# Performance work log

Measured on AMD Instinct MI355X. Metric: run time of the kernel, lower is better.

## Reference

```python
import jax, jax.numpy as jnp
import numpy as np

DIM = 2048
Q_C = 1536
KV_C = 512
H = 16
DH = 128
DR = 64
EPS = 1e-6
B = 4
T = 2048


def rmsnorm(x, g, eps=EPS):
    var = jnp.mean(x * x, axis=-1, keepdims=True)
    return x * jax.lax.rsqrt(var + eps) * g


def apply_rope(x, freqs_cis):
    # x: [B, t, h, d]; freqs_cis: [t, d//2, 2] (cos, sin)
    xs = x.reshape(*x.shape[:-1], -1, 2)
    x1, x2 = xs[..., 0], xs[..., 1]
    cos = freqs_cis[None, :, None, :, 0]
    sin = freqs_cis[None, :, None, :, 1]
    o1 = x1 * cos - x2 * sin
    o2 = x1 * sin + x2 * cos
    return jnp.stack([o1, o2], axis=-1).reshape(x.shape)


def setup_inputs() -> dict:
    key = jax.random.key(0)
    ks = jax.random.split(key, 12)
    s = lambda fan_in: 1.0 / np.sqrt(fan_in)
    inp = {}
    inp["x"] = jax.random.normal(ks[0], (B, T, DIM), dtype=jnp.float32)
    inp["start_pos"] = 0
    # rotary frequencies for decoupled dim
    inv_freq = 1.0 / (10000.0 ** (np.arange(0, DR, 2, dtype=np.float32) / DR))
    angles = np.arange(T, dtype=np.float32)[:, None] * inv_freq[None, :]  # [T, DR//2]
    inp["freqs_cis"] = jnp.asarray(np.stack([np.cos(angles), np.sin(angles)], axis=-1))
    # causal additive mask
    neg = jnp.float32(-1e9)
    inp["mask"] = jnp.where(jnp.tril(jnp.ones((T, T), dtype=bool)), 0.0, neg).astype(jnp.float32)
    # weights stored as (in, out)
    inp["W_dq"] = jax.random.normal(ks[1], (DIM, Q_C), dtype=jnp.float32) * s(DIM)
    inp["W_uq"] = jax.random.normal(ks[2], (Q_C, H * DH), dtype=jnp.float32) * s(Q_C)
    inp["W_dkv"] = jax.random.normal(ks[3], (DIM, KV_C), dtype=jnp.float32) * s(DIM)
    inp["W_uk"] = jax.random.normal(ks[4], (KV_C, H * DH), dtype=jnp.float32) * s(KV_C)
    inp["W_uv"] = jax.random.normal(ks[5], (KV_C, H * DH), dtype=jnp.float32) * s(KV_C)
    inp["W_qr"] = jax.random.normal(ks[6], (Q_C, H * DR), dtype=jnp.float32) * s(Q_C)
    inp["W_kr"] = jax.random.normal(ks[7], (DIM, DR), dtype=jnp.float32) * s(DIM)
    inp["W_o"] = jax.random.normal(ks[8], (H * DH, DIM), dtype=jnp.float32) * s(H * DH)
    inp["g_q"] = jnp.ones((Q_C,), dtype=jnp.float32)
    inp["g_kv"] = jnp.ones((KV_C,), dtype=jnp.float32)
    return inp


def reference(x, start_pos, freqs_cis, mask, W_dq, W_uq, W_dkv, W_uk, W_uv, W_qr, W_kr, W_o, g_q, g_kv):
    Bc, t, _ = x.shape
    q_c = rmsnorm(x @ W_dq, g_q)            # [B, t, Q_C]
    kv_c = rmsnorm(x @ W_dkv, g_kv)         # [B, t, KV_C]
    q_rope = (q_c @ W_qr).reshape(Bc, t, H, DR)
    q_rope = apply_rope(q_rope, freqs_cis)
    k_rope = apply_rope((x @ W_kr)[:, :, None, :], freqs_cis)  # [B, t, 1, DR]
    k_rope = jnp.broadcast_to(k_rope, (Bc, t, H, DR))
    q = (q_c @ W_uq).reshape(Bc, t, H, DH)
    k = (kv_c @ W_uk).reshape(Bc, t, H, DH)
    v = (kv_c @ W_uv).reshape(Bc, t, H, DH)
    q = jnp.concatenate([q, q_rope], axis=-1)  # [B, t, H, DH+DR]
    k = jnp.concatenate([k, k_rope], axis=-1)
    scale = 1.0 / np.sqrt(DH + DR)
    scores = jnp.einsum("bqhd,bkhd->bhqk", q, k) * scale + mask
    probs = jax.nn.softmax(scores, axis=-1)
    out = jnp.einsum("bhqk,bkhd->bqhd", probs, v).reshape(Bc, t, H * DH)
    return out @ W_o
```

## Files before the change

kernel.cpp:

```cpp
#include <hip/hip_runtime.h>
#include <cstdint>
#include <cstddef>

typedef unsigned short u16;
typedef __attribute__((ext_vector_type(8))) short s8v;
typedef __attribute__((ext_vector_type(4))) float f4v;

__device__ __forceinline__ float bf2f(u16 u) {
  union { unsigned u; float f; } v; v.u = ((unsigned)u) << 16; return v.f;
}
__device__ __forceinline__ u16 f2bf(float f) {
  union { float f; unsigned u; } v; v.f = f;
  unsigned r = v.u + 0x7FFFu + ((v.u >> 16) & 1u);
  return (u16)(r >> 16);
}

__device__ __forceinline__ void async16(u16* lds, const u16* g) {
  __builtin_amdgcn_global_load_lds((const __attribute__((address_space(1))) void*)g,
                                   (__attribute__((address_space(3))) void*)lds,
                                   16, 0, 0);
}

__global__ __launch_bounds__(256) void k_f32_to_bf16(const float* __restrict__ in,
                                                     u16* __restrict__ out, int n8) {
  int i = blockIdx.x * 256 + threadIdx.x;
  if (i >= n8) return;
  const float4* p = (const float4*)(in + (size_t)i * 8);
  float4 a = p[0], b = p[1];
  s8v ov;
  ov[0] = (short)f2bf(a.x); ov[1] = (short)f2bf(a.y);
  ov[2] = (short)f2bf(a.z); ov[3] = (short)f2bf(a.w);
  ov[4] = (short)f2bf(b.x); ov[5] = (short)f2bf(b.y);
  ov[6] = (short)f2bf(b.z); ov[7] = (short)f2bf(b.w);
  *(s8v*)(out + (size_t)i * 8) = ov;
}

__global__ __launch_bounds__(256) void k_transpose_bf16(const float* __restrict__ W,
                                                        u16* __restrict__ Wt, int K, int N) {
  __shared__ float tile[32][33];
  int n0 = blockIdx.x * 32, k0 = blockIdx.y * 32;
  int tx = threadIdx.x & 31, ty = threadIdx.x >> 5;
#pragma unroll
  for (int i = 0; i < 32; i += 8)
    tile[ty + i][tx] = W[(size_t)(k0 + ty + i) * N + n0 + tx];
  __syncthreads();
#pragma unroll
  for (int i = 0; i < 32; i += 8)
    Wt[(size_t)(n0 + ty + i) * K + k0 + tx] = f2bf(tile[tx][ty + i]);
}

template <int BM, int BN, int WVM, int WVN, typename OutT, bool REMAP>
__global__ __launch_bounds__(256, 2) void k_gemm_bt(const u16* __restrict__ A,
                                                    const u16* __restrict__ Bt,
                                                    OutT* __restrict__ C,
                                                    int M, int N, int K, int ldc) {
  constexpr int FM = BM / WVM / 16, FN = BN / WVN / 16;
  __shared__ __align__(16) u16 As[BM * 32];
  __shared__ __align__(16) u16 Bs[BN * 32];
  const int tid = threadIdx.x, wv = tid >> 6, ln = tid & 63;
  const int lo = ln & 15, hi = ln >> 4;
  const int wr = wv / WVN, wc = wv % WVN;

  int nwg = gridDim.x, bid = blockIdx.x;
  int s = (bid & 7) * (nwg >> 3) + (bid >> 3);
  int gm = M / BM;
  int m0 = (s % gm) * BM, n0 = (s / gm) * BN;

  f4v acc[FM][FN] = {};

  for (int k0 = 0; k0 < K; k0 += 32) {
    __syncthreads();
#pragma unroll
    for (int i = 0; i < BM / 64; i++) {
      int r = i * 64 + wv * 16 + (ln >> 2);
      async16(&As[(i * 64 + wv * 16) * 32],
              A + (size_t)(m0 + r) * K + k0 + (ln & 3) * 8);
    }
#pragma unroll
    for (int i = 0; i < BN / 64; i++) {
      int r = i * 64 + wv * 16 + (ln >> 2);
      async16(&Bs[(i * 64 + wv * 16) * 32],
              Bt + (size_t)(n0 + r) * K + k0 + (ln & 3) * 8);
    }
    __syncthreads();

    s8v af[FM], bf[FN];
#pragma unroll
    for (int m = 0; m < FM; m++)
      af[m] = *(const s8v*)&As[(wr * FM * 16 + m * 16 + lo) * 32 + hi * 8];
#pragma unroll
    for (int n = 0; n < FN; n++)
      bf[n] = *(const s8v*)&Bs[(wc * FN * 16 + n * 16 + lo) * 32 + hi * 8];
#pragma unroll
    for (int m = 0; m < FM; m++)
#pragma unroll
      for (int n = 0; n < FN; n++)
        acc[m][n] = __builtin_amdgcn_mfma_f32_16x16x32_bf16(af[m], bf[n], acc[m][n], 0, 0, 0);
  }

#pragma unroll
  for (int m = 0; m < FM; m++)
#pragma unroll
    for (int n = 0; n < FN; n++)
#pragma unroll
      for (int j = 0; j < 4; j++) {
        int row = m0 + wr * FM * 16 + m * 16 + hi * 4 + j;
        int col = n0 + wc * FN * 16 + n * 16 + lo;
        int dc = REMAP ? ((col >> 7) * 192 + (col & 127)) : col;
        float v = acc[m][n][j];
        if constexpr (sizeof(OutT) == 2)
          C[(size_t)row * ldc + dc] = (OutT)f2bf(v);
        else
          C[(size_t)row * ldc + dc] = (OutT)v;
      }
}

__global__ __launch_bounds__(256) void k_rmsnorm(u16* __restrict__ buf,
                                                 const float* __restrict__ g, int C) {
  int row = blockIdx.x;
  u16* p = buf + (size_t)row * C;
  int tid = threadIdx.x;
  bool act = tid * 8 < C;
  float x[8];
  float ss = 0.f;
  if (act) {
    s8v v = *(const s8v*)(p + tid * 8);
#pragma unroll
    for (int i = 0; i < 8; i++) { float xi = bf2f((u16)v[i]); x[i] = xi; ss += xi * xi; }
  }
#pragma unroll
  for (int off = 1; off < 64; off <<= 1) ss += __shfl_xor(ss, off);
  __shared__ float red[4];
  if ((tid & 63) == 0) red[tid >> 6] = ss;
  __syncthreads();
  float sc = rsqrtf((red[0] + red[1] + red[2] + red[3]) / (float)C + 1e-6f);
  if (act) {
    s8v ov;
#pragma unroll
    for (int i = 0; i < 8; i++) ov[i] = (short)f2bf(x[i] * sc * g[tid * 8 + i]);
    *(s8v*)(p + tid * 8) = ov;
  }
}

__global__ __launch_bounds__(256) void k_rope_q(const u16* __restrict__ qr,
                                                const float* __restrict__ freqs,
                                                u16* __restrict__ qbuf) {
  int idx = blockIdx.x * 256 + threadIdx.x;
  int r = idx >> 4, h = idx & 15;
  int t = r & 2047;
  const u16* src = qr + (size_t)r * 1024 + h * 64;
  u16* dst = qbuf + (size_t)r * 3072 + h * 192 + 128;
  const float* fc = freqs + (size_t)t * 64;
  u16 in[64], out[64];
#pragma unroll
  for (int c = 0; c < 8; c++) {
    s8v vv = *(const s8v*)(src + c * 8);
#pragma unroll
    for (int e = 0; e < 8; e++) in[c * 8 + e] = (u16)vv[e];
  }
#pragma unroll
  for (int i = 0; i < 32; i++) {
    float x1 = bf2f(in[2 * i]), x2 = bf2f(in[2 * i + 1]);
    float co = fc[2 * i], si = fc[2 * i + 1];
    out[2 * i] = f2bf(x1 * co - x2 * si);
    out[2 * i + 1] = f2bf(x1 * si + x2 * co);
  }
#pragma unroll
  for (int c = 0; c < 8; c++) {
    s8v ov;
#pragma unroll
    for (int e = 0; e < 8; e++) ov[e] = (short)out[c * 8 + e];
    *(s8v*)(dst + c * 8) = ov;
  }
}

__global__ __launch_bounds__(256) void k_rope_k(const u16* __restrict__ kr,
                                                const float* __restrict__ freqs,
                                                u16* __restrict__ kbuf) {
  int idx = blockIdx.x * 256 + threadIdx.x;
  int r = idx >> 4, h = idx & 15;
  int t = r & 2047;
  const u16* src = kr + (size_t)r * 64;
  u16* dst = kbuf + (size_t)r * 3072 + h * 192 + 128;
  const float* fc = freqs + (size_t)t * 64;
  u16 in[64], out[64];
#pragma unroll
  for (int c = 0; c < 8; c++) {
    s8v vv = *(const s8v*)(src + c * 8);
#pragma unroll
    for (int e = 0; e < 8; e++) in[c * 8 + e] = (u16)vv[e];
  }
#pragma unroll
  for (int i = 0; i < 32; i++) {
    float x1 = bf2f(in[2 * i]), x2 = bf2f(in[2 * i + 1]);
    float co = fc[2 * i], si = fc[2 * i + 1];
    out[2 * i] = f2bf(x1 * co - x2 * si);
    out[2 * i + 1] = f2bf(x1 * si + x2 * co);
  }
#pragma unroll
  for (int c = 0; c < 8; c++) {
    s8v ov;
#pragma unroll
    for (int e = 0; e < 8; e++) ov[e] = (short)out[c * 8 + e];
    *(s8v*)(dst + c * 8) = ov;
  }
}

__global__ __launch_bounds__(256) void k_transpose_v(const u16* __restrict__ vtmp,
                                                     u16* __restrict__ vt) {
  __shared__ __align__(16) u16 tile[64][72];
  int r0 = blockIdx.x * 64, c0 = blockIdx.y * 64;
  int b = r0 >> 11, t0 = r0 & 2047;
  int h = c0 >> 7, d0 = c0 & 127;
  int tid = threadIdx.x;
  int ci = (tid & 7) * 8, ri = tid >> 3;
#pragma unroll
  for (int i = 0; i < 2; i++)
    *(s8v*)&tile[ri + 32 * i][ci] =
        *(const s8v*)(vtmp + (size_t)(r0 + ri + 32 * i) * 2048 + c0 + ci);
  __syncthreads();
  int tx = tid & 7, rr = tid >> 3;
#pragma unroll
  for (int i = 0; i < 2; i++) {
    int dr = rr + 32 * i;
    s8v ov;
#pragma unroll
    for (int e = 0; e < 8; e++) ov[e] = (short)tile[tx * 8 + e][dr];
    *(s8v*)(vt + (size_t)((b * 16 + h) * 128 + d0 + dr) * 2048 + t0 + tx * 8) = ov;
  }
}

__global__ __launch_bounds__(256, 3) void k_attn(const u16* __restrict__ Q,
                                                 const u16* __restrict__ K,
                                                 const u16* __restrict__ V,
                                                 u16* __restrict__ O) {
  __shared__ __align__(16) u16 Ks[64 * 192];
  __shared__ __align__(16) u16 Vs[128 * 64];
  __shared__ __align__(16) u16 p_lds[4][16 * 88];
  int bid = blockIdx.x;
  int lw = (bid & 7) * 256 + (bid >> 3);
  int qt = 31 - (lw & 31), h = (lw >> 5) & 15, b = lw >> 9;
  int tid = threadIdx.x, wv = tid >> 6, ln = tid & 63;
  int lo = ln & 15, hi = ln >> 4, lo7 = lo & 7;
  int qb = qt * 64 + wv * 16;

  const u16* qptr = Q + (size_t)(b * 2048 + qb + lo) * 3072 + h * 192 + hi * 8;
  s8v qf[6];
#pragma unroll
  for (int ks = 0; ks < 6; ks++) qf[ks] = *(const s8v*)(qptr + ks * 32);

  f4v Oa[8] = {};
  float m_r[4], l_r[4];
#pragma unroll
  for (int j = 0; j < 4; j++) { m_r[j] = -3e38f; l_r[j] = 0.f; }
  const float scale = 0.07216878364870323f;

  const u16* kg = K + (size_t)(b * 2048) * 3072 + h * 192;
  const u16* vg = V + (size_t)((b * 16 + h) * 128) * 2048;
  int kgo[6], klo[6];
#pragma unroll
  for (int i = 0; i < 6; i++) {
    int id = i * 256 + tid, r = id / 24, c = id % 24;
    kgo[i] = r * 3072 + c * 8;
    klo[i] = r * 192 + (c ^ (r & 7)) * 8;
  }
  int vgo[4], vlo[4];
#pragma unroll
  for (int i = 0; i < 4; i++) {
    int id = i * 256 + tid, r = id >> 3, c = id & 7;
    vgo[i] = r * 2048 + c * 8;
    vlo[i] = r * 64 + (c ^ (r & 7)) * 8;
  }

  u16* pl = p_lds[wv];
  int last = (qb + 15) >> 6;
  s8v kreg[6], vreg[4];

#pragma unroll
  for (int i = 0; i < 6; i++) kreg[i] = *(const s8v*)(kg + kgo[i]);
#pragma unroll
  for (int i = 0; i < 4; i++) vreg[i] = *(const s8v*)(vg + vgo[i]);
#pragma unroll
  for (int i = 0; i < 6; i++) *(s8v*)&Ks[klo[i]] = kreg[i];
#pragma unroll
  for (int i = 0; i < 4; i++) *(s8v*)&Vs[vlo[i]] = vreg[i];
  __syncthreads();

  for (int t = 0; t <= last; t++) {
    int kv0 = t * 64;
    if (t < last) {
      size_t ksh = (size_t)(kv0 + 64) * 3072;
#pragma unroll
      for (int i = 0; i < 6; i++) kreg[i] = *(const s8v*)(kg + ksh + kgo[i]);
#pragma unroll
      for (int i = 0; i < 4; i++) vreg[i] = *(const s8v*)(vg + (kv0 + 64) + vgo[i]);
    }

    f4v S[4] = {};
#pragma unroll
    for (int ks = 0; ks < 6; ks++)
#pragma unroll
      for (int nf = 0; nf < 4; nf++) {
        s8v kf = *(const s8v*)&Ks[(nf * 16 + lo) * 192 + (((ks * 4 + hi) ^ lo7) * 8)];
        S[nf] = __builtin_amdgcn_mfma_f32_16x16x32_bf16(qf[ks], kf, S[nf], 0, 0, 0);
      }

    float p[4][4], tmax[4];
#pragma unroll
    for (int j = 0; j < 4; j++) tmax[j] = -3e38f;
    bool diag = (t == last);
#pragma unroll
    for (int nf = 0; nf < 4; nf++)
#pragma unroll
      for (int j = 0; j < 4; j++) {
        float sv = S[nf][j] * scale;
        if (diag && (kv0 + nf * 16 + lo > qb + hi * 4 + j)) sv = -3e38f;
        p[nf][j] = sv;
        tmax[j] = fmaxf(tmax[j], sv);
      }
#pragma unroll
    for (int off = 1; off < 16; off <<= 1)
#pragma unroll
      for (int j = 0; j < 4; j++) tmax[j] = fmaxf(tmax[j], __shfl_xor(tmax[j], off));
    float fj[4], ts[4];
#pragma unroll
    for (int j = 0; j < 4; j++) {
      float nm = fmaxf(m_r[j], tmax[j]);
      fj[j] = __expf(m_r[j] - nm);
      m_r[j] = nm;
      ts[j] = 0.f;
    }
#pragma unroll
    for (int nf = 0; nf < 4; nf++)
#pragma unroll
      for (int j = 0; j < 4; j++) {
        float pv = __expf(p[nf][j] - m_r[j]);
        p[nf][j] = pv;
        ts[j] += pv;
      }
#pragma unroll
    for (int off = 1; off < 16; off <<= 1)
#pragma unroll
      for (int j = 0; j < 4; j++) ts[j] += __shfl_xor(ts[j], off);
#pragma unroll
    for (int j = 0; j < 4; j++) l_r[j] = l_r[j] * fj[j] + ts[j];
#pragma unroll
    for (int df = 0; df < 8; df++)
#pragma unroll
      for (int j = 0; j < 4; j++) Oa[df][j] *= fj[j];

#pragma unroll
    for (int nf = 0; nf < 4; nf++)
#pragma unroll
      for (int j = 0; j < 4; j++)
        pl[(hi * 4 + j) * 88 + nf * 16 + lo] = f2bf(p[nf][j]);

#pragma unroll
    for (int ks2 = 0; ks2 < 2; ks2++) {
      s8v pa = *(const s8v*)&pl[lo * 88 + ks2 * 32 + hi * 8];
#pragma unroll
      for (int df = 0; df < 8; df++) {
        s8v vf = *(const s8v*)&Vs[(df * 16 + lo) * 64 + (((ks2 * 4 + hi) ^ lo7) * 8)];
        Oa[df] = __builtin_amdgcn_mfma_f32_16x16x32_bf16(pa, vf, Oa[df], 0, 0, 0);
      }
    }

    __syncthreads();
    if (t < last) {
#pragma unroll
      for (int i = 0; i < 6; i++) *(s8v*)&Ks[klo[i]] = kreg[i];
#pragma unroll
      for (int i = 0; i < 4; i++) *(s8v*)&Vs[vlo[i]] = vreg[i];
      __syncthreads();
    }
  }

#pragma unroll
  for (int j = 0; j < 4; j++) {
    float inv = 1.0f / l_r[j];
    u16* orow = O + (size_t)(b * 2048 + qb + hi * 4 + j) * 2048 + h * 128;
#pragma unroll
    for (int df = 0; df < 8; df++) orow[df * 16 + lo] = f2bf(Oa[df][j] * inv);
  }
}

extern "C" void kernel_launch(void* const* d_in, const int* in_sizes, int n_in,
                              void* d_out, int out_size, void* d_ws, size_t ws_size,
                              hipStream_t stream) {
  (void)in_sizes; (void)n_in; (void)out_size; (void)ws_size;
  const float* x     = (const float*)d_in[0];
  const float* freqs = (const float*)d_in[2];
  const float* W_dq  = (const float*)d_in[4];
  const float* W_uq  = (const float*)d_in[5];
  const float* W_dkv = (const float*)d_in[6];
  const float* W_uk  = (const float*)d_in[7];
  const float* W_uv  = (const float*)d_in[8];
  const float* W_qr  = (const float*)d_in[9];
  const float* W_kr  = (const float*)d_in[10];
  const float* W_o   = (const float*)d_in[11];
  const float* g_q   = (const float*)d_in[12];
  const float* g_kv  = (const float*)d_in[13];
  float* out = (float*)d_out;

  const int M = 8192;
  char* w = (char*)d_ws;
  auto alloc = [&](size_t n) { char* p = w; w += (n + 255) & ~(size_t)255; return p; };

  u16* xb     = (u16*)alloc((size_t)M * 2048 * 2);
  u16* wdq    = (u16*)alloc((size_t)1536 * 2048 * 2);
  u16* wuq    = (u16*)alloc((size_t)2048 * 1536 * 2);
  u16* wdkv   = (u16*)alloc((size_t)512 * 2048 * 2);
  u16* wuk    = (u16*)alloc((size_t)2048 * 512 * 2);
  u16* wuv    = (u16*)alloc((size_t)2048 * 512 * 2);
  u16* wqr    = (u16*)alloc((size_t)1024 * 1536 * 2);
  u16* wkr    = (u16*)alloc((size_t)64 * 2048 * 2);
  u16* wo     = (u16*)alloc((size_t)2048 * 2048 * 2);
  u16* q_c    = (u16*)alloc((size_t)M * 1536 * 2);
  u16* kv_c   = (u16*)alloc((size_t)M * 512 * 2);
  u16* qr_raw = (u16*)alloc((size_t)M * 1024 * 2);
  u16* kr_raw = (u16*)alloc((size_t)M * 64 * 2);
  u16* qbuf   = (u16*)alloc((size_t)M * 3072 * 2);
  u16* kbuf   = (u16*)alloc((size_t)M * 3072 * 2);
  u16* vt     = (u16*)alloc((size_t)M * 2048 * 2);
  u16* vtmp = xb;
  u16* aout = xb;

  k_f32_to_bf16<<<M * 2048 / 8 / 256, 256, 0, stream>>>(x, xb, M * 2048 / 8);
  k_transpose_bf16<<<dim3(1536 / 32, 2048 / 32), 256, 0, stream>>>(W_dq, wdq, 2048, 1536);
  k_transpose_bf16<<<dim3(2048 / 32, 1536 / 32), 256, 0, stream>>>(W_uq, wuq, 1536, 2048);
  k_transpose_bf16<<<dim3(512 / 32, 2048 / 32), 256, 0, stream>>>(W_dkv, wdkv, 2048, 512);
  k_transpose_bf16<<<dim3(2048 / 32, 512 / 32), 256, 0, stream>>>(W_uk, wuk, 512, 2048);
  k_transpose_bf16<<<dim3(2048 / 32, 512 / 32), 256, 0, stream>>>(W_uv, wuv, 512, 2048);
  k_transpose_bf16<<<dim3(1024 / 32, 1536 / 32), 256, 0, stream>>>(W_qr, wqr, 1536, 1024);
  k_transpose_bf16<<<dim3(64 / 32, 2048 / 32), 256, 0, stream>>>(W_kr, wkr, 2048, 64);
  k_transpose_bf16<<<dim3(2048 / 32, 2048 / 32), 256, 0, stream>>>(W_o, wo, 2048, 2048);

  k_gemm_bt<128, 128, 2, 2, u16, false><<<(M / 128) * (1536 / 128), 256, 0, stream>>>(
      xb, wdq, q_c, M, 1536, 2048, 1536);
  k_rmsnorm<<<M, 256, 0, stream>>>(q_c, g_q, 1536);
  k_gemm_bt<128, 128, 2, 2, u16, false><<<(M / 128) * (512 / 128), 256, 0, stream>>>(
      xb, wdkv, kv_c, M, 512, 2048, 512);
  k_rmsnorm<<<M, 256, 0, stream>>>(kv_c, g_kv, 512);

  k_gemm_bt<128, 128, 2, 2, u16, true><<<(M / 128) * (2048 / 128), 256, 0, stream>>>(
      q_c, wuq, qbuf, M, 2048, 1536, 3072);
  k_gemm_bt<128, 128, 2, 2, u16, false><<<(M / 128) * (1024 / 128), 256, 0, stream>>>(
      q_c, wqr, qr_raw, M, 1024, 1536, 1024);
  k_rope_q<<<M * 16 / 256, 256, 0, stream>>>(qr_raw, freqs, qbuf);

  k_gemm_bt<128, 128, 2, 2, u16, true><<<(M / 128) * (2048 / 128), 256, 0, stream>>>(
      kv_c, wuk, kbuf, M, 2048, 512, 3072);
  k_gemm_bt<128, 64, 4, 1, u16, false><<<(M / 128) * (64 / 64), 256, 0, stream>>>(
      xb, wkr, kr_raw, M, 64, 2048, 64);
  k_rope_k<<<M * 16 / 256, 256, 0, stream>>>(kr_raw, freqs, kbuf);

  k_gemm_bt<128, 128, 2, 2, u16, false><<<(M / 128) * (2048 / 128), 256, 0, stream>>>(
      kv_c, wuv, vtmp, M, 2048, 512, 2048);
  k_transpose_v<<<dim3(M / 64, 2048 / 64), 256, 0, stream>>>(vtmp, vt);

  k_attn<<<4 * 16 * 32, 256, 0, stream>>>(qbuf, kbuf, vt, aout);

  k_gemm_bt<128, 128, 2, 2, float, false><<<(M / 128) * (2048 / 128), 256, 0, stream>>>(
      aout, wo, out, M, 2048, 2048, 2048);
}
```

Measured before the change: 839.0 us.

## Fuse sibling projection GEMMs and add lazy softmax rescaling in attention

Sibling projection GEMMs that share an input are merged into one launch by laying out their transposed weights next to each other (W_dq+W_dkv, W_uq+W_qr, W_uk+W_uv). A split-column epilogue routes each output half to its own buffer, which cuts launches and re-reads of the shared input. The attention kernel folds the scale into an exp2 multiplier, skips the rescale of the running max and accumulator unless the tile max grows past a threshold, and defers the row-sum reduction to the end. It also raises wave priority around the MFMA blocks. RMSNorm now launches with exactly C/8 threads, and bf16 conversion uses the library intrinsic; the lazy rescale can lose some precision if scores vary widely.

```diff
diff --git a/kernel.cpp b/kernel.cpp
--- a/kernel.cpp
+++ b/kernel.cpp
@@ -1,4 +1,5 @@
 #include <hip/hip_runtime.h>
+#include <hip/hip_bf16.h>
 #include <cstdint>
 #include <cstddef>
 
@@ -10,9 +11,8 @@
   union { unsigned u; float f; } v; v.u = ((unsigned)u) << 16; return v.f;
 }
 __device__ __forceinline__ u16 f2bf(float f) {
-  union { float f; unsigned u; } v; v.f = f;
-  unsigned r = v.u + 0x7FFFu + ((v.u >> 16) & 1u);
-  return (u16)(r >> 16);
+  __hip_bfloat16 h = __float2bfloat16(f);
+  return *reinterpret_cast<u16*>(&h);
 }
 
 __device__ __forceinline__ void async16(u16* lds, const u16* g) {
@@ -49,11 +49,12 @@
     Wt[(size_t)(n0 + ty + i) * K + k0 + tx] = f2bf(tile[tx][ty + i]);
 }
 
-template <int BM, int BN, int WVM, int WVN, typename OutT, bool REMAP>
-__global__ __launch_bounds__(256, 2) void k_gemm_bt(const u16* __restrict__ A,
-                                                    const u16* __restrict__ Bt,
-                                                    OutT* __restrict__ C,
-                                                    int M, int N, int K, int ldc) {
+template <int BM, int BN, int WVM, int WVN, int EPI>
+__global__ __launch_bounds__(256, 2) void k_gemm(const u16* __restrict__ A,
+                                                 const u16* __restrict__ Bt,
+                                                 void* __restrict__ C0v,
+                                                 void* __restrict__ C1v,
+                                                 int M, int N, int K, int split) {
   constexpr int FM = BM / WVM / 16, FN = BN / WVN / 16;
   __shared__ __align__(16) u16 As[BM * 32];
   __shared__ __align__(16) u16 Bs[BN * 32];
@@ -98,6 +99,7 @@
         acc[m][n] = __builtin_amdgcn_mfma_f32_16x16x32_bf16(af[m], bf[n], acc[m][n], 0, 0, 0);
   }
 
+  bool second = (n0 >= split);
 #pragma unroll
   for (int m = 0; m < FM; m++)
 #pragma unroll
@@ -106,40 +108,45 @@
       for (int j = 0; j < 4; j++) {
         int row = m0 + wr * FM * 16 + m * 16 + hi * 4 + j;
         int col = n0 + wc * FN * 16 + n * 16 + lo;
-        int dc = REMAP ? ((col >> 7) * 192 + (col & 127)) : col;
         float v = acc[m][n][j];
-        if constexpr (sizeof(OutT) == 2)
-          C[(size_t)row * ldc + dc] = (OutT)f2bf(v);
-        else
-          C[(size_t)row * ldc + dc] = (OutT)v;
+        if constexpr (EPI == 0) {
+          ((u16*)C0v)[(size_t)row * N + col] = f2bf(v);
+        } else if constexpr (EPI == 1) {
+          ((float*)C0v)[(size_t)row * N + col] = v;
+        } else if constexpr (EPI == 2) {
+          if (second) ((u16*)C1v)[(size_t)row * 512 + (col - 1536)] = f2bf(v);
+          else        ((u16*)C0v)[(size_t)row * 1536 + col] = f2bf(v);
+        } else if constexpr (EPI == 3) {
+          if (second) ((u16*)C1v)[(size_t)row * 1024 + (col - 2048)] = f2bf(v);
+          else        ((u16*)C0v)[(size_t)row * 3072 + (col >> 7) * 192 + (col & 127)] = f2bf(v);
+        } else {
+          if (second) ((u16*)C1v)[(size_t)row * 2048 + (col - 2048)] = f2bf(v);
+          else        ((u16*)C0v)[(size_t)row * 3072 + (col >> 7) * 192 + (col & 127)] = f2bf(v);
+        }
       }
 }
 
-__global__ __launch_bounds__(256) void k_rmsnorm(u16* __restrict__ buf,
-                                                 const float* __restrict__ g, int C) {
+__global__ void k_rmsnorm(u16* __restrict__ buf, const float* __restrict__ g, int C) {
   int row = blockIdx.x;
   u16* p = buf + (size_t)row * C;
   int tid = threadIdx.x;
-  bool act = tid * 8 < C;
   float x[8];
   float ss = 0.f;
-  if (act) {
-    s8v v = *(const s8v*)(p + tid * 8);
-#pragma unroll
-    for (int i = 0; i < 8; i++) { float xi = bf2f((u16)v[i]); x[i] = xi; ss += xi * xi; }
-  }
+  s8v v = *(const s8v*)(p + tid * 8);
+#pragma unroll
+  for (int i = 0; i < 8; i++) { float xi = bf2f((u16)v[i]); x[i] = xi; ss += xi * xi; }
 #pragma unroll
   for (int off = 1; off < 64; off <<= 1) ss += __shfl_xor(ss, off);
   __shared__ float red[4];
+  if (tid < 4) red[tid] = 0.f;
+  __syncthreads();
   if ((tid & 63) == 0) red[tid >> 6] = ss;
   __syncthreads();
   float sc = rsqrtf((red[0] + red[1] + red[2] + red[3]) / (float)C + 1e-6f);
-  if (act) {
-    s8v ov;
-#pragma unroll
-    for (int i = 0; i < 8; i++) ov[i] = (short)f2bf(x[i] * sc * g[tid * 8 + i]);
-    *(s8v*)(p + tid * 8) = ov;
-  }
+  s8v ov;
+#pragma unroll
+  for (int i = 0; i < 8; i++) ov[i] = (short)f2bf(x[i] * sc * g[tid * 8 + i]);
+  *(s8v*)(p + tid * 8) = ov;
 }
 
 __global__ __launch_bounds__(256) void k_rope_q(const u16* __restrict__ qr,
@@ -250,10 +257,11 @@
   for (int ks = 0; ks < 6; ks++) qf[ks] = *(const s8v*)(qptr + ks * 32);
 
   f4v Oa[8] = {};
-  float m_r[4], l_r[4];
-#pragma unroll
-  for (int j = 0; j < 4; j++) { m_r[j] = -3e38f; l_r[j] = 0.f; }
-  const float scale = 0.07216878364870323f;
+  float m_r[4], lpart[4];
+#pragma unroll
+  for (int j = 0; j < 4; j++) { m_r[j] = -3e38f; lpart[j] = 0.f; }
+  const float sl2 = 0.07216878364870323f * 1.44269504f;
+  const float THRU = 11.5f / sl2;
 
   const u16* kg = K + (size_t)(b * 2048) * 3072 + h * 192;
   const u16* vg = V + (size_t)((b * 16 + h) * 128) * 2048;
@@ -297,6 +305,7 @@
     }
 
     f4v S[4] = {};
+    __builtin_amdgcn_s_setprio(1);
 #pragma unroll
     for (int ks = 0; ks < 6; ks++)
 #pragma unroll
@@ -304,50 +313,56 @@
         s8v kf = *(const s8v*)&Ks[(nf * 16 + lo) * 192 + (((ks * 4 + hi) ^ lo7) * 8)];
         S[nf] = __builtin_amdgcn_mfma_f32_16x16x32_bf16(qf[ks], kf, S[nf], 0, 0, 0);
       }
+    __builtin_amdgcn_s_setprio(0);
 
     float p[4][4], tmax[4];
 #pragma unroll
     for (int j = 0; j < 4; j++) tmax[j] = -3e38f;
-    bool diag = (t == last);
+    if (t == last) {
+#pragma unroll
+      for (int nf = 0; nf < 4; nf++)
+#pragma unroll
+        for (int j = 0; j < 4; j++) {
+          float sv = S[nf][j];
+          if (kv0 + nf * 16 + lo > qb + hi * 4 + j) sv = -3e38f;
+          p[nf][j] = sv;
+          tmax[j] = fmaxf(tmax[j], sv);
+        }
+    } else {
+#pragma unroll
+      for (int nf = 0; nf < 4; nf++)
+#pragma unroll
+        for (int j = 0; j < 4; j++) {
+          p[nf][j] = S[nf][j];
+          tmax[j] = fmaxf(tmax[j], S[nf][j]);
+        }
+    }
+    bool need = false;
+#pragma unroll
+    for (int j = 0; j < 4; j++) need = need || (tmax[j] > m_r[j] + THRU);
+    if (__any(need)) {
+#pragma unroll
+      for (int off = 1; off < 16; off <<= 1)
+#pragma unroll
+        for (int j = 0; j < 4; j++) tmax[j] = fmaxf(tmax[j], __shfl_xor(tmax[j], off));
+#pragma unroll
+      for (int j = 0; j < 4; j++) {
+        float nm = fmaxf(m_r[j], tmax[j]);
+        float fj = exp2f((m_r[j] - nm) * sl2);
+        m_r[j] = nm;
+        lpart[j] *= fj;
+#pragma unroll
+        for (int df = 0; df < 8; df++) Oa[df][j] *= fj;
+      }
+    }
 #pragma unroll
     for (int nf = 0; nf < 4; nf++)
 #pragma unroll
       for (int j = 0; j < 4; j++) {
-        float sv = S[nf][j] * scale;
-        if (diag && (kv0 + nf * 16 + lo > qb + hi * 4 + j)) sv = -3e38f;
-        p[nf][j] = sv;
-        tmax[j] = fmaxf(tmax[j], sv);
+        float pv = exp2f((p[nf][j] - m_r[j]) * sl2);
+        p[nf][j] = pv;
+        lpart[j] += pv;
       }
-#pragma unroll
-    for (int off = 1; off < 16; off <<= 1)
-#pragma unroll
-      for (int j = 0; j < 4; j++) tmax[j] = fmaxf(tmax[j], __shfl_xor(tmax[j], off));
-    float fj[4], ts[4];
-#pragma unroll
-    for (int j = 0; j < 4; j++) {
-      float nm = fmaxf(m_r[j], tmax[j]);
-      fj[j] = __expf(m_r[j] - nm);
-      m_r[j] = nm;
-      ts[j] = 0.f;
-    }
-#pragma unroll
-    for (int nf = 0; nf < 4; nf++)
-#pragma unroll
-      for (int j = 0; j < 4; j++) {
-        float pv = __expf(p[nf][j] - m_r[j]);
-        p[nf][j] = pv;
-        ts[j] += pv;
-      }
-#pragma unroll
-    for (int off = 1; off < 16; off <<= 1)
-#pragma unroll
-      for (int j = 0; j < 4; j++) ts[j] += __shfl_xor(ts[j], off);
-#pragma unroll
-    for (int j = 0; j < 4; j++) l_r[j] = l_r[j] * fj[j] + ts[j];
-#pragma unroll
-    for (int df = 0; df < 8; df++)
-#pragma unroll
-      for (int j = 0; j < 4; j++) Oa[df][j] *= fj[j];
 
 #pragma unroll
     for (int nf = 0; nf < 4; nf++)
@@ -355,6 +370,7 @@
       for (int j = 0; j < 4; j++)
         pl[(hi * 4 + j) * 88 + nf * 16 + lo] = f2bf(p[nf][j]);
 
+    __builtin_amdgcn_s_setprio(1);
 #pragma unroll
     for (int ks2 = 0; ks2 < 2; ks2++) {
       s8v pa = *(const s8v*)&pl[lo * 88 + ks2 * 32 + hi * 8];
@@ -364,6 +380,7 @@
         Oa[df] = __builtin_amdgcn_mfma_f32_16x16x32_bf16(pa, vf, Oa[df], 0, 0, 0);
       }
     }
+    __builtin_amdgcn_s_setprio(0);
 
     __syncthreads();
     if (t < last) {
@@ -376,8 +393,13 @@
   }
 
 #pragma unroll
+  for (int off = 1; off < 16; off <<= 1)
+#pragma unroll
+    for (int j = 0; j < 4; j++) lpart[j] += __shfl_xor(lpart[j], off);
+
+#pragma unroll
   for (int j = 0; j < 4; j++) {
-    float inv = 1.0f / l_r[j];
+    float inv = 1.0f / lpart[j];
     u16* orow = O + (size_t)(b * 2048 + qb + hi * 4 + j) * 2048 + h * 128;
 #pragma unroll
     for (int df = 0; df < 8; df++) orow[df * 16 + lo] = f2bf(Oa[df][j] * inv);
@@ -408,11 +430,11 @@
 
   u16* xb     = (u16*)alloc((size_t)M * 2048 * 2);
   u16* wdq    = (u16*)alloc((size_t)1536 * 2048 * 2);
+  u16* wdkv   = (u16*)alloc((size_t)512 * 2048 * 2);
   u16* wuq    = (u16*)alloc((size_t)2048 * 1536 * 2);
-  u16* wdkv   = (u16*)alloc((size_t)512 * 2048 * 2);
+  u16* wqr    = (u16*)alloc((size_t)1024 * 1536 * 2);
   u16* wuk    = (u16*)alloc((size_t)2048 * 512 * 2);
   u16* wuv    = (u16*)alloc((size_t)2048 * 512 * 2);
-  u16* wqr    = (u16*)alloc((size_t)1024 * 1536 * 2);
   u16* wkr    = (u16*)alloc((size_t)64 * 2048 * 2);
   u16* wo     = (u16*)alloc((size_t)2048 * 2048 * 2);
   u16* q_c    = (u16*)alloc((size_t)M * 1536 * 2);
@@ -427,39 +449,33 @@
 
   k_f32_to_bf16<<<M * 2048 / 8 / 256, 256, 0, stream>>>(x, xb, M * 2048 / 8);
   k_transpose_bf16<<<dim3(1536 / 32, 2048 / 32), 256, 0, stream>>>(W_dq, wdq, 2048, 1536);
+  k_transpose_bf16<<<dim3(512 / 32, 2048 / 32), 256, 0, stream>>>(W_dkv, wdkv, 2048, 512);
   k_transpose_bf16<<<dim3(2048 / 32, 1536 / 32), 256, 0, stream>>>(W_uq, wuq, 1536, 2048);
-  k_transpose_bf16<<<dim3(512 / 32, 2048 / 32), 256, 0, stream>>>(W_dkv, wdkv, 2048, 512);
+  k_transpose_bf16<<<dim3(1024 / 32, 1536 / 32), 256, 0, stream>>>(W_qr, wqr, 1536, 1024);
   k_transpose_bf16<<<dim3(2048 / 32, 512 / 32), 256, 0, stream>>>(W_uk, wuk, 512, 2048);
   k_transpose_bf16<<<dim3(2048 / 32, 512 / 32), 256, 0, stream>>>(W_uv, wuv, 512, 2048);
-  k_transpose_bf16<<<dim3(1024 / 32, 1536 / 32), 256, 0, stream>>>(W_qr, wqr, 1536, 1024);
   k_transpose_bf16<<<dim3(64 / 32, 2048 / 32), 256, 0, stream>>>(W_kr, wkr, 2048, 64);
   k_transpose_bf16<<<dim3(2048 / 32, 2048 / 32), 256, 0, stream>>>(W_o, wo, 2048, 2048);
 
-  k_gemm_bt<128, 128, 2, 2, u16, false><<<(M / 128) * (1536 / 128), 256, 0, stream>>>(
-      xb, wdq, q_c, M, 1536, 2048, 1536);
-  k_rmsnorm<<<M, 256, 0, stream>>>(q_c, g_q, 1536);
-  k_gemm_bt<128, 128, 2, 2, u16, false><<<(M / 128) * (512 / 128), 256, 0, stream>>>(
-      xb, wdkv, kv_c, M, 512, 2048, 512);
-  k_rmsnorm<<<M, 256, 0, stream>>>(kv_c, g_kv, 512);
-
-  k_gemm_bt<128, 128, 2, 2, u16, true><<<(M / 128) * (2048 / 128), 256, 0, stream>>>(
-      q_c, wuq, qbuf, M, 2048, 1536, 3072);
-  k_gemm_bt<128, 128, 2, 2, u16, false><<<(M / 128) * (1024 / 128), 256, 0, stream>>>(
-      q_c, wqr, qr_raw, M, 1024, 1536, 1024);
+  k_gemm<128, 128, 2, 2, 2><<<(M / 128) * (2048 / 128), 256, 0, stream>>>(
+      xb, wdq, q_c, kv_c, M, 2048, 2048, 1536);
+  k_rmsnorm<<<M, 192, 0, stream>>>(q_c, g_q, 1536);
+  k_rmsnorm<<<M, 64, 0, stream>>>(kv_c, g_kv, 512);
+
+  k_gemm<128, 128, 2, 2, 3><<<(M / 128) * (3072 / 128), 256, 0, stream>>>(
+      q_c, wuq, qbuf, qr_raw, M, 3072, 1536, 2048);
   k_rope_q<<<M * 16 / 256, 256, 0, stream>>>(qr_raw, freqs, qbuf);
 
-  k_gemm_bt<128, 128, 2, 2, u16, true><<<(M / 128) * (2048 / 128), 256, 0, stream>>>(
-      kv_c, wuk, kbuf, M, 2048, 512, 3072);
-  k_gemm_bt<128, 64, 4, 1, u16, false><<<(M / 128) * (64 / 64), 256, 0, stream>>>(
-      xb, wkr, kr_raw, M, 64, 2048, 64);
+  k_gemm<128, 64, 4, 1, 0><<<(M / 128) * (64 / 64), 256, 0, stream>>>(
+      xb, wkr, kr_raw, nullptr, M, 64, 2048, 1 << 30);
   k_rope_k<<<M * 16 / 256, 256, 0, stream>>>(kr_raw, freqs, kbuf);
 
-  k_gemm_bt<128, 128, 2, 2, u16, false><<<(M / 128) * (2048 / 128), 256, 0, stream>>>(
-      kv_c, wuv, vtmp, M, 2048, 512, 2048);
+  k_gemm<128, 128, 2, 2, 4><<<(M / 128) * (4096 / 128), 256, 0, stream>>>(
+      kv_c, wuk, kbuf, vtmp, M, 4096, 512, 2048);
   k_transpose_v<<<dim3(M / 64, 2048 / 64), 256, 0, stream>>>(vtmp, vt);
 
   k_attn<<<4 * 16 * 32, 256, 0, stream>>>(qbuf, kbuf, vt, aout);
 
-  k_gemm_bt<128, 128, 2, 2, float, false><<<(M / 128) * (2048 / 128), 256, 0, stream>>>(
-      aout, wo, out, M, 2048, 2048, 2048);
-}
+  k_gemm<128, 128, 2, 2, 1><<<(M / 128) * (2048 / 128), 256, 0, stream>>>(
+      aout, wo, out, nullptr, M, 2048, 2048, 1 << 30);
+}
```

After: 855.2 us. About the same (+1.9%).
